# Performance work log

Measured on AMD Instinct MI355X. Metric: run time of the kernel, lower is better.

Reference implementation:

```python
import jax, jax.numpy as jnp
import numpy as np

BANDWIDTH = 1.0  # init kwarg: bandwidth; sphere mode -> var_s = gamma = bandwidth
LOG2PI = float(np.log(2.0 * np.pi))


def setup_inputs() -> dict:
    key = jax.random.key(0)
    k1, k2, k3, k4 = jax.random.split(key, 4)
    x = jax.random.normal(k1, (4096, 256), dtype=jnp.float32)
    y = jax.random.normal(k2, (4096, 128), dtype=jnp.float32)
    x_s = jax.random.normal(k3, (8192, 256), dtype=jnp.float32)
    y_s = jax.random.normal(k4, (8192, 128), dtype=jnp.float32)
    return {"x": x, "y": y, "x_s": x_s, "y_s": y_s}


def _sq_dists(a, b):
    # ||a_i - b_j||^2 via GEMM expansion: (batch, num_s)
    a2 = jnp.sum(a * a, axis=-1)[:, None]
    b2 = jnp.sum(b * b, axis=-1)[None, :]
    return a2 + b2 - 2.0 * jnp.einsum("bd,sd->bs", a, b)


def reference(x, y, x_s, y_s):
    x_dim = x.shape[-1]
    y_dim = y.shape[-1]
    var_s = BANDWIDTH
    gamma = BANDWIDTH
    logA_x = x_dim * (LOG2PI + jnp.log(jnp.float32(var_s)))
    logA_y = y_dim * (LOG2PI + jnp.log(jnp.float32(gamma)))

    sdx = _sq_dists(x, x_s) / var_s  # (batch, num_s)
    sdy = _sq_dists(y, y_s) / gamma  # (batch, num_s)

    E_log_pxy = jax.nn.logsumexp(-0.5 * (logA_x + logA_y + sdx + sdy), axis=-1)
    E_log_px = jax.nn.logsumexp(-0.5 * (logA_x + sdx), axis=-1)
    E_log_py = jax.nn.logsumexp(-0.5 * (logA_y + sdy), axis=-1)
    return jnp.mean(E_log_pxy - E_log_px - E_log_py)
```

## Files before the change

kernel.cpp:

```cpp
#include <hip/hip_runtime.h>
#include <hip/hip_bf16.h>
#include <stdint.h>

#define B_N 4096
#define S_N 8192
#define KX  256
#define KY  128
#define BM 128
#define BN 128

typedef __bf16 bf16x8 __attribute__((ext_vector_type(8)));
typedef float  f32x4  __attribute__((ext_vector_type(4)));

#define OFF_XH   ((size_t)0)
#define OFF_YH   ((size_t)2097152)
#define OFF_SXH  ((size_t)3145728)
#define OFF_SYH  ((size_t)7340032)
#define OFF_NX   ((size_t)9437184)
#define OFF_NY   (OFF_NX + 16384)
#define OFF_NSX  (OFF_NY + 16384)
#define OFF_NSY  (OFF_NSX + 32768)
#define OFF_PART (OFF_NSY + 32768)
#define OFF_BSUM (OFF_PART + (size_t)3*64*4096*2*4)

__device__ __forceinline__ void gl2lds16(const void* g, void* l) {
  typedef const __attribute__((address_space(1))) unsigned int* gp_t;
  typedef __attribute__((address_space(3))) unsigned int* lp_t;
  __builtin_amdgcn_global_load_lds((gp_t)g, (lp_t)l, 16, 0, 0);
}

__device__ __forceinline__ unsigned short f2bf(float f) {
  unsigned u = __builtin_bit_cast(unsigned, f);
  return (unsigned short)((u + 0x7fffu + ((u >> 16) & 1u)) >> 16);
}

__global__ __launch_bounds__(256) void conv_all(const float* __restrict__ x,
                                                const float* __restrict__ y,
                                                const float* __restrict__ xs,
                                                const float* __restrict__ ys,
                                                char* __restrict__ ws) {
  int b    = blockIdx.x;
  int wave = threadIdx.x >> 6;
  int lane = threadIdx.x & 63;
  if (b == 0 && threadIdx.x < 2) ((unsigned*)(ws + OFF_BSUM))[threadIdx.x] = 0u;
  const float* src; unsigned short* hi; float* nrm;
  int K, r0;
  if (b < 256) {
    src = x;  hi = (unsigned short*)(ws + OFF_XH);
    nrm = (float*)(ws + OFF_NX);  K = 256; r0 = b * 16 + wave * 4;
  } else if (b < 512) {
    src = y;  hi = (unsigned short*)(ws + OFF_YH);
    nrm = (float*)(ws + OFF_NY);  K = 128; r0 = (b - 256) * 16 + wave * 4;
  } else if (b < 1024) {
    src = xs; hi = (unsigned short*)(ws + OFF_SXH);
    nrm = (float*)(ws + OFF_NSX); K = 256; r0 = (b - 512) * 16 + wave * 4;
  } else {
    src = ys; hi = (unsigned short*)(ws + OFF_SYH);
    nrm = (float*)(ws + OFF_NSY); K = 128; r0 = (b - 1024) * 16 + wave * 4;
  }
  if (K == 256) {
    float4 v[4];
    #pragma unroll
    for (int j = 0; j < 4; ++j)
      v[j] = ((const float4*)(src + (size_t)(r0 + j) * 256))[lane];
    #pragma unroll
    for (int j = 0; j < 4; ++j) {
      float vv[4] = {v[j].x, v[j].y, v[j].z, v[j].w};
      ushort4 h4;
      unsigned short* hp = (unsigned short*)&h4;
      float acc = 0.f;
      #pragma unroll
      for (int k = 0; k < 4; ++k) {
        hp[k] = f2bf(vv[k]);
        acc = fmaf(vv[k], vv[k], acc);
      }
      ((ushort4*)(hi + (size_t)(r0 + j) * 256))[lane] = h4;
      #pragma unroll
      for (int o = 32; o > 0; o >>= 1) acc += __shfl_down(acc, o);
      if (lane == 0) nrm[r0 + j] = acc;
    }
  } else {
    float2 v[4];
    #pragma unroll
    for (int j = 0; j < 4; ++j)
      v[j] = ((const float2*)(src + (size_t)(r0 + j) * 128))[lane];
    #pragma unroll
    for (int j = 0; j < 4; ++j) {
      float vv[2] = {v[j].x, v[j].y};
      ushort2 h2;
      unsigned short* hp = (unsigned short*)&h2;
      float acc = 0.f;
      #pragma unroll
      for (int k = 0; k < 2; ++k) {
        hp[k] = f2bf(vv[k]);
        acc = fmaf(vv[k], vv[k], acc);
      }
      ((ushort2*)(hi + (size_t)(r0 + j) * 128))[lane] = h2;
      #pragma unroll
      for (int o = 32; o > 0; o >>= 1) acc += __shfl_down(acc, o);
      if (lane == 0) nrm[r0 + j] = acc;
    }
  }
}

__global__ __launch_bounds__(512, 4) void mie_main(const char* __restrict__ ws,
                                                   float* __restrict__ part) {
  __shared__ __align__(16) char smem[65536];

  const int tid  = threadIdx.x;
  const int lane = tid & 63;
  const int wave = tid >> 6;
  const int c    = lane & 15;
  const int q    = lane >> 4;
  const int wm   = wave >> 1;
  const int wn   = wave & 1;

  const int b     = blockIdx.x;
  const int xcd   = b & 7;
  const int w     = b >> 3;
  const int bm_t  = w & 31;
  const int sn_t  = xcd * 8 + (w >> 5);
  const int bm0   = bm_t * BM;
  const int sn0   = sn_t * BN;

  const char* xh  = ws + OFF_XH;
  const char* yh  = ws + OFF_YH;
  const char* sxh = ws + OFF_SXH;
  const char* syh = ws + OFF_SYH;
  const float* nx  = (const float*)(ws + OFF_NX);
  const float* ny  = (const float*)(ws + OFF_NY);
  const float* nsx = (const float*)(ws + OFF_NSX);
  const float* nsy = (const float*)(ws + OFF_NSY);

  const int r  = tid >> 2;
  const int sg = (tid & 3) ^ ((r >> 1) & 3);
  const char* aXp = xh  + (size_t)(bm0 + r) * 512 + sg * 16;
  const char* aYp = yh  + (size_t)(bm0 + r) * 256 + sg * 16;
  const char* bXp = sxh + (size_t)(sn0 + r) * 512 + sg * 16;
  const char* bYp = syh + (size_t)(sn0 + r) * 256 + sg * 16;
  char* sdst = smem + wave * 1024;

  const int slot  = (q ^ ((c >> 1) & 3)) * 16;
  const int aoff0 = (wm * 32 +  0 + c) * 64 + slot;
  const int aoff1 = (wm * 32 + 16 + c) * 64 + slot;
  const int boff0 = (wn * 64 +  0 + c) * 64 + slot;
  const int boff1 = (wn * 64 + 16 + c) * 64 + slot;
  const int boff2 = (wn * 64 + 32 + c) * 64 + slot;
  const int boff3 = (wn * 64 + 48 + c) * 64 + slot;

  f32x4 accx[2][4], accy[2][4];
  #pragma unroll
  for (int i = 0; i < 2; ++i)
    #pragma unroll
    for (int j = 0; j < 4; ++j) {
      accx[i][j] = (f32x4){0.f,0.f,0.f,0.f};
      accy[i][j] = (f32x4){0.f,0.f,0.f,0.f};
    }

#define STAGE(kc) do {                                                      \
    const char* _sa; const char* _sb;                                       \
    if ((kc) < 8) { _sa = aXp + (kc) * 64;       _sb = bXp + (kc) * 64; }   \
    else          { _sa = aYp + ((kc) - 8) * 64; _sb = bYp + ((kc) - 8) * 64; } \
    char* _d = sdst + ((kc) & 3) * 16384;                                   \
    gl2lds16(_sa, _d);                                                      \
    gl2lds16(_sb, _d + 8192);                                               \
  } while (0)

#define MFMA8(ACC, A0, A1, B0, B1, B2, B3) do {                                   \
    ACC[0][0] = __builtin_amdgcn_mfma_f32_16x16x32_bf16(A0, B0, ACC[0][0], 0,0,0); \
    ACC[0][1] = __builtin_amdgcn_mfma_f32_16x16x32_bf16(A0, B1, ACC[0][1], 0,0,0); \
    ACC[0][2] = __builtin_amdgcn_mfma_f32_16x16x32_bf16(A0, B2, ACC[0][2], 0,0,0); \
    ACC[0][3] = __builtin_amdgcn_mfma_f32_16x16x32_bf16(A0, B3, ACC[0][3], 0,0,0); \
    ACC[1][0] = __builtin_amdgcn_mfma_f32_16x16x32_bf16(A1, B0, ACC[1][0], 0,0,0); \
    ACC[1][1] = __builtin_amdgcn_mfma_f32_16x16x32_bf16(A1, B1, ACC[1][1], 0,0,0); \
    ACC[1][2] = __builtin_amdgcn_mfma_f32_16x16x32_bf16(A1, B2, ACC[1][2], 0,0,0); \
    ACC[1][3] = __builtin_amdgcn_mfma_f32_16x16x32_bf16(A1, B3, ACC[1][3], 0,0,0); \
  } while (0)

#define ITER(kc, vm, ACC) do {                                              \
    asm volatile("s_waitcnt vmcnt(" #vm ")" ::: "memory");                  \
    __builtin_amdgcn_s_barrier();                                           \
    asm volatile("" ::: "memory");                                          \
    const char* _base = smem + ((kc) & 3) * 16384;                          \
    bf16x8 _A0 = *(const bf16x8*)(_base + aoff0);                           \
    bf16x8 _A1 = *(const bf16x8*)(_base + aoff1);                           \
    bf16x8 _B0 = *(const bf16x8*)(_base + 8192 + boff0);                    \
    bf16x8 _B1 = *(const bf16x8*)(_base + 8192 + boff1);                    \
    bf16x8 _B2 = *(const bf16x8*)(_base + 8192 + boff2);                    \
    bf16x8 _B3 = *(const bf16x8*)(_base + 8192 + boff3);                    \
    if ((kc) + 3 < 12) STAGE((kc) + 3);                                     \
    __builtin_amdgcn_s_setprio(1);                                          \
    MFMA8(ACC, _A0, _A1, _B0, _B1, _B2, _B3);                               \
    __builtin_amdgcn_s_setprio(0);                                          \
  } while (0)

  STAGE(0); STAGE(1); STAGE(2);

  ITER(0, 4, accx);  ITER(1, 4, accx);  ITER(2, 4, accx);  ITER(3, 4, accx);
  ITER(4, 4, accx);  ITER(5, 4, accx);  ITER(6, 4, accx);  ITER(7, 4, accx);
  ITER(8, 4, accy);  ITER(9, 4, accy);  ITER(10, 2, accy); ITER(11, 0, accy);

#undef ITER
#undef MFMA8
#undef STAGE

  __syncthreads();

  float hxv[2][4], hyv[2][4];
  #pragma unroll
  for (int i = 0; i < 2; ++i)
    #pragma unroll
    for (int rr4 = 0; rr4 < 4; ++rr4) {
      int rr = bm0 + wm * 32 + i * 16 + q * 4 + rr4;
      hxv[i][rr4] = -0.5f * nx[rr];
      hyv[i][rr4] = -0.5f * ny[rr];
    }
  float hsxv[4], hsyv[4];
  #pragma unroll
  for (int j = 0; j < 4; ++j) {
    int cc = sn0 + wn * 64 + j * 16 + c;
    hsxv[j] = -0.5f * nsx[cc];
    hsyv[j] = -0.5f * nsy[cc];
  }

  float2* xch2 = (float2*)smem;
  #pragma unroll
  for (int i = 0; i < 2; ++i) {
    #pragma unroll
    for (int rr4 = 0; rr4 < 4; ++rr4) {
      float vx[4], vy[4];
      #pragma unroll
      for (int j = 0; j < 4; ++j) {
        vx[j] = accx[i][j][rr4] + hxv[i][rr4] + hsxv[j];
        vy[j] = accy[i][j][rr4] + hyv[i][rr4] + hsyv[j];
      }
      int rl = wm * 32 + i * 16 + q * 4 + rr4;
      #pragma unroll
      for (int st = 0; st < 3; ++st) {
        float v0 = (st == 0) ? vx[0] + vy[0] : (st == 1 ? vx[0] : vy[0]);
        float v1 = (st == 0) ? vx[1] + vy[1] : (st == 1 ? vx[1] : vy[1]);
        float v2 = (st == 0) ? vx[2] + vy[2] : (st == 1 ? vx[2] : vy[2]);
        float v3 = (st == 0) ? vx[3] + vy[3] : (st == 1 ? vx[3] : vy[3]);
        float m = fmaxf(fmaxf(v0, v1), fmaxf(v2, v3));
        float s = __expf(v0 - m) + __expf(v1 - m) + __expf(v2 - m) + __expf(v3 - m);
        float mo = __shfl_xor(m, 8);
        float so = __shfl_xor(s, 8);
        float nm = fmaxf(m, mo);
        float ns = s * __expf(m - nm) + so * __expf(mo - nm);
        if (c < 8) xch2[(st * 128 + rl) * 16 + wn * 8 + c] = (float2){nm, ns};
      }
    }
  }
  __syncthreads();

  if (tid < 384) {
    int st = tid >> 7;
    int rl = tid & 127;
    const float2* row = xch2 + (st * 128 + rl) * 16;
    int p0 = rl & 15;
    float2 a = row[p0];
    float m = a.x, s = a.y;
    #pragma unroll
    for (int p = 1; p < 16; ++p) {
      float2 e = row[(p0 + p) & 15];
      float nm = fmaxf(m, e.x);
      s = s * __expf(m - nm) + e.y * __expf(e.x - nm);
      m = nm;
    }
    size_t idx = ((size_t)st * 64 + sn_t) * B_N + (bm0 + rl);
    ((float2*)part)[idx] = (float2){m, s};
  }
}

__global__ __launch_bounds__(256) void fin_all(const float* __restrict__ part,
                                               char* __restrict__ ws,
                                               float* __restrict__ out) {
  __shared__ float2 lds[3][4][64];
  int tid  = threadIdx.x;
  int wave = tid >> 6;
  int lane = tid & 63;
  int row  = blockIdx.x * 64 + lane;
  #pragma unroll
  for (int j = 0; j < 3; ++j) {
    float m = -__builtin_inff(), s = 0.f;
    #pragma unroll
    for (int pp = 0; pp < 16; ++pp) {
      int p = wave * 16 + pp;
      float2 a = ((const float2*)part)[((size_t)j * 64 + p) * B_N + row];
      float nm = fmaxf(m, a.x);
      s = s * __expf(m - nm) + a.y * __expf(a.x - nm);
      m = nm;
    }
    lds[j][wave][lane] = (float2){m, s};
  }
  __syncthreads();
  if (wave == 0) {
    float v[3];
    #pragma unroll
    for (int j = 0; j < 3; ++j) {
      float m = -__builtin_inff(), s = 0.f;
      #pragma unroll
      for (int u = 0; u < 4; ++u) {
        float2 a = lds[j][u][lane];
        float nm = fmaxf(m, a.x);
        s = s * __expf(m - nm) + a.y * __expf(a.x - nm);
        m = nm;
      }
      v[j] = m + __logf(s);
    }
    float local = v[0] - v[1] - v[2];
    #pragma unroll
    for (int o = 32; o > 0; o >>= 1) local += __shfl_down(local, o);
    if (lane == 0) {
      unsigned* done = (unsigned*)(ws + OFF_BSUM);
      float*    fsum = (float*)(done + 1);
      atomicAdd(fsum, local);
      __threadfence();
      unsigned old = atomicAdd(done, 1u);
      if (old == 63u) {
        __threadfence();
        float tot = atomicAdd(fsum, 0.0f);
        out[0] = tot * (1.0f / (float)B_N);
      }
    }
  }
}

extern "C" void kernel_launch(void* const* d_in, const int* in_sizes, int n_in,
                              void* d_out, int out_size, void* d_ws, size_t ws_size,
                              hipStream_t stream) {
  (void)in_sizes; (void)n_in; (void)out_size; (void)ws_size;
  const float* x  = (const float*)d_in[0];
  const float* y  = (const float*)d_in[1];
  const float* xs = (const float*)d_in[2];
  const float* ys = (const float*)d_in[3];
  char* ws = (char*)d_ws;

  conv_all<<<1536, 256, 0, stream>>>(x, y, xs, ys, ws);
  mie_main<<<2048, 512, 0, stream>>>(ws, (float*)(ws + OFF_PART));
  fin_all<<<B_N / 64, 256, 0, stream>>>((const float*)(ws + OFF_PART), ws, (float*)d_out);
}
```

Measured before the change: 129.5 us.

## Enlarge main-kernel tile to 256x128 rows for more operand reuse

Doubles the batch-row tile of the fused dual-GEMM/logsumexp kernel from 128 to 256, so each wave computes a 64x64 sub-tile with 16 MFMAs per k-step instead of 8. Staging, LDS layout, the wait counts, the epilogue reduction and the grid size are all reworked to match. This cuts global and LDS traffic per MFMA and halves the block count. The cost is more accumulator registers, 96KB of LDS and an occupancy target lowered to two blocks per CU, which reduces latency hiding.

```diff
diff --git a/kernel.cpp b/kernel.cpp
--- a/kernel.cpp
+++ b/kernel.cpp
@@ -6,7 +6,7 @@
 #define S_N 8192
 #define KX  256
 #define KY  128
-#define BM 128
+#define BM 256
 #define BN 128
 
 typedef __bf16 bf16x8 __attribute__((ext_vector_type(8)));
@@ -103,9 +103,9 @@
   }
 }
 
-__global__ __launch_bounds__(512, 4) void mie_main(const char* __restrict__ ws,
+__global__ __launch_bounds__(512, 2) void mie_main(const char* __restrict__ ws,
                                                    float* __restrict__ part) {
-  __shared__ __align__(16) char smem[65536];
+  __shared__ __align__(16) char smem[98304];
 
   const int tid  = threadIdx.x;
   const int lane = tid & 63;
@@ -118,8 +118,8 @@
   const int b     = blockIdx.x;
   const int xcd   = b & 7;
   const int w     = b >> 3;
-  const int bm_t  = w & 31;
-  const int sn_t  = xcd * 8 + (w >> 5);
+  const int bm_t  = w & 15;
+  const int sn_t  = xcd * 8 + (w >> 4);
   const int bm0   = bm_t * BM;
   const int sn0   = sn_t * BN;
 
@@ -132,25 +132,24 @@
   const float* nsx = (const float*)(ws + OFF_NSX);
   const float* nsy = (const float*)(ws + OFF_NSY);
 
-  const int r  = tid >> 2;
-  const int sg = (tid & 3) ^ ((r >> 1) & 3);
-  const char* aXp = xh  + (size_t)(bm0 + r) * 512 + sg * 16;
-  const char* aYp = yh  + (size_t)(bm0 + r) * 256 + sg * 16;
-  const char* bXp = sxh + (size_t)(sn0 + r) * 512 + sg * 16;
-  const char* bYp = syh + (size_t)(sn0 + r) * 256 + sg * 16;
+  const int rA = tid >> 2;
+  const int sg = (tid & 3) ^ ((rA >> 1) & 3);
+  const char* aXp = xh  + (size_t)(bm0 + rA) * 512 + sg * 16;
+  const char* aYp = yh  + (size_t)(bm0 + rA) * 256 + sg * 16;
+  const char* bXp = sxh + (size_t)(sn0 + rA) * 512 + sg * 16;
+  const char* bYp = syh + (size_t)(sn0 + rA) * 256 + sg * 16;
   char* sdst = smem + wave * 1024;
 
-  const int slot  = (q ^ ((c >> 1) & 3)) * 16;
-  const int aoff0 = (wm * 32 +  0 + c) * 64 + slot;
-  const int aoff1 = (wm * 32 + 16 + c) * 64 + slot;
-  const int boff0 = (wn * 64 +  0 + c) * 64 + slot;
-  const int boff1 = (wn * 64 + 16 + c) * 64 + slot;
-  const int boff2 = (wn * 64 + 32 + c) * 64 + slot;
-  const int boff3 = (wn * 64 + 48 + c) * 64 + slot;
-
-  f32x4 accx[2][4], accy[2][4];
-  #pragma unroll
-  for (int i = 0; i < 2; ++i)
+  const int slot = (q ^ ((c >> 1) & 3)) * 16;
+  int aoff[4], boff[4];
+  #pragma unroll
+  for (int i = 0; i < 4; ++i) aoff[i] = (wm * 64 + i * 16 + c) * 64 + slot;
+  #pragma unroll
+  for (int j = 0; j < 4; ++j) boff[j] = 16384 + (wn * 64 + j * 16 + c) * 64 + slot;
+
+  f32x4 accx[4][4], accy[4][4];
+  #pragma unroll
+  for (int i = 0; i < 4; ++i)
     #pragma unroll
     for (int j = 0; j < 4; ++j) {
       accx[i][j] = (f32x4){0.f,0.f,0.f,0.f};
@@ -158,15 +157,19 @@
     }
 
 #define STAGE(kc) do {                                                      \
-    const char* _sa; const char* _sb;                                       \
-    if ((kc) < 8) { _sa = aXp + (kc) * 64;       _sb = bXp + (kc) * 64; }   \
-    else          { _sa = aYp + ((kc) - 8) * 64; _sb = bYp + ((kc) - 8) * 64; } \
-    char* _d = sdst + ((kc) & 3) * 16384;                                   \
-    gl2lds16(_sa, _d);                                                      \
-    gl2lds16(_sb, _d + 8192);                                               \
+    char* _d = sdst + ((kc) & 3) * 24576;                                   \
+    if ((kc) < 8) {                                                         \
+      gl2lds16(aXp + (kc) * 64,         _d);                                \
+      gl2lds16(aXp + 65536 + (kc) * 64, _d + 8192);                         \
+      gl2lds16(bXp + (kc) * 64,         _d + 16384);                        \
+    } else {                                                                \
+      gl2lds16(aYp + ((kc) - 8) * 64,         _d);                          \
+      gl2lds16(aYp + 32768 + ((kc) - 8) * 64, _d + 8192);                   \
+      gl2lds16(bYp + ((kc) - 8) * 64,         _d + 16384);                  \
+    }                                                                       \
   } while (0)
 
-#define MFMA8(ACC, A0, A1, B0, B1, B2, B3) do {                                   \
+#define MFMA16(ACC, A0, A1, A2, A3, B0, B1, B2, B3) do {                          \
     ACC[0][0] = __builtin_amdgcn_mfma_f32_16x16x32_bf16(A0, B0, ACC[0][0], 0,0,0); \
     ACC[0][1] = __builtin_amdgcn_mfma_f32_16x16x32_bf16(A0, B1, ACC[0][1], 0,0,0); \
     ACC[0][2] = __builtin_amdgcn_mfma_f32_16x16x32_bf16(A0, B2, ACC[0][2], 0,0,0); \
@@ -175,46 +178,47 @@
     ACC[1][1] = __builtin_amdgcn_mfma_f32_16x16x32_bf16(A1, B1, ACC[1][1], 0,0,0); \
     ACC[1][2] = __builtin_amdgcn_mfma_f32_16x16x32_bf16(A1, B2, ACC[1][2], 0,0,0); \
     ACC[1][3] = __builtin_amdgcn_mfma_f32_16x16x32_bf16(A1, B3, ACC[1][3], 0,0,0); \
+    ACC[2][0] = __builtin_amdgcn_mfma_f32_16x16x32_bf16(A2, B0, ACC[2][0], 0,0,0); \
+    ACC[2][1] = __builtin_amdgcn_mfma_f32_16x16x32_bf16(A2, B1, ACC[2][1], 0,0,0); \
+    ACC[2][2] = __builtin_amdgcn_mfma_f32_16x16x32_bf16(A2, B2, ACC[2][2], 0,0,0); \
+    ACC[2][3] = __builtin_amdgcn_mfma_f32_16x16x32_bf16(A2, B3, ACC[2][3], 0,0,0); \
+    ACC[3][0] = __builtin_amdgcn_mfma_f32_16x16x32_bf16(A3, B0, ACC[3][0], 0,0,0); \
+    ACC[3][1] = __builtin_amdgcn_mfma_f32_16x16x32_bf16(A3, B1, ACC[3][1], 0,0,0); \
+    ACC[3][2] = __builtin_amdgcn_mfma_f32_16x16x32_bf16(A3, B2, ACC[3][2], 0,0,0); \
+    ACC[3][3] = __builtin_amdgcn_mfma_f32_16x16x32_bf16(A3, B3, ACC[3][3], 0,0,0); \
   } while (0)
 
 #define ITER(kc, vm, ACC) do {                                              \
     asm volatile("s_waitcnt vmcnt(" #vm ")" ::: "memory");                  \
     __builtin_amdgcn_s_barrier();                                           \
     asm volatile("" ::: "memory");                                          \
-    const char* _base = smem + ((kc) & 3) * 16384;                          \
-    bf16x8 _A0 = *(const bf16x8*)(_base + aoff0);                           \
-    bf16x8 _A1 = *(const bf16x8*)(_base + aoff1);                           \
-    bf16x8 _B0 = *(const bf16x8*)(_base + 8192 + boff0);                    \
-    bf16x8 _B1 = *(const bf16x8*)(_base + 8192 + boff1);                    \
-    bf16x8 _B2 = *(const bf16x8*)(_base + 8192 + boff2);                    \
-    bf16x8 _B3 = *(const bf16x8*)(_base + 8192 + boff3);                    \
+    const char* _base = smem + ((kc) & 3) * 24576;                          \
+    bf16x8 _A0 = *(const bf16x8*)(_base + aoff[0]);                         \
+    bf16x8 _A1 = *(const bf16x8*)(_base + aoff[1]);                         \
+    bf16x8 _A2 = *(const bf16x8*)(_base + aoff[2]);                         \
+    bf16x8 _A3 = *(const bf16x8*)(_base + aoff[3]);                         \
+    bf16x8 _B0 = *(const bf16x8*)(_base + boff[0]);                         \
+    bf16x8 _B1 = *(const bf16x8*)(_base + boff[1]);                         \
+    bf16x8 _B2 = *(const bf16x8*)(_base + boff[2]);                         \
+    bf16x8 _B3 = *(const bf16x8*)(_base + boff[3]);                         \
     if ((kc) + 3 < 12) STAGE((kc) + 3);                                     \
     __builtin_amdgcn_s_setprio(1);                                          \
-    MFMA8(ACC, _A0, _A1, _B0, _B1, _B2, _B3);                               \
+    MFMA16(ACC, _A0, _A1, _A2, _A3, _B0, _B1, _B2, _B3);                    \
     __builtin_amdgcn_s_setprio(0);                                          \
   } while (0)
 
   STAGE(0); STAGE(1); STAGE(2);
 
-  ITER(0, 4, accx);  ITER(1, 4, accx);  ITER(2, 4, accx);  ITER(3, 4, accx);
-  ITER(4, 4, accx);  ITER(5, 4, accx);  ITER(6, 4, accx);  ITER(7, 4, accx);
-  ITER(8, 4, accy);  ITER(9, 4, accy);  ITER(10, 2, accy); ITER(11, 0, accy);
+  ITER(0, 6, accx);  ITER(1, 6, accx);  ITER(2, 6, accx);  ITER(3, 6, accx);
+  ITER(4, 6, accx);  ITER(5, 6, accx);  ITER(6, 6, accx);  ITER(7, 6, accx);
+  ITER(8, 6, accy);  ITER(9, 6, accy);  ITER(10, 3, accy); ITER(11, 0, accy);
 
 #undef ITER
-#undef MFMA8
+#undef MFMA16
 #undef STAGE
 
   __syncthreads();
 
-  float hxv[2][4], hyv[2][4];
-  #pragma unroll
-  for (int i = 0; i < 2; ++i)
-    #pragma unroll
-    for (int rr4 = 0; rr4 < 4; ++rr4) {
-      int rr = bm0 + wm * 32 + i * 16 + q * 4 + rr4;
-      hxv[i][rr4] = -0.5f * nx[rr];
-      hyv[i][rr4] = -0.5f * ny[rr];
-    }
   float hsxv[4], hsyv[4];
   #pragma unroll
   for (int j = 0; j < 4; ++j) {
@@ -225,16 +229,18 @@
 
   float2* xch2 = (float2*)smem;
   #pragma unroll
-  for (int i = 0; i < 2; ++i) {
+  for (int i = 0; i < 4; ++i) {
     #pragma unroll
     for (int rr4 = 0; rr4 < 4; ++rr4) {
+      int rowg = wm * 64 + i * 16 + q * 4 + rr4;
+      float hx = -0.5f * nx[bm0 + rowg];
+      float hy = -0.5f * ny[bm0 + rowg];
       float vx[4], vy[4];
       #pragma unroll
       for (int j = 0; j < 4; ++j) {
-        vx[j] = accx[i][j][rr4] + hxv[i][rr4] + hsxv[j];
-        vy[j] = accy[i][j][rr4] + hyv[i][rr4] + hsyv[j];
-      }
-      int rl = wm * 32 + i * 16 + q * 4 + rr4;
+        vx[j] = accx[i][j][rr4] + hx + hsxv[j];
+        vy[j] = accy[i][j][rr4] + hy + hsyv[j];
+      }
       #pragma unroll
       for (int st = 0; st < 3; ++st) {
         float v0 = (st == 0) ? vx[0] + vy[0] : (st == 1 ? vx[0] : vy[0]);
@@ -247,16 +253,16 @@
         float so = __shfl_xor(s, 8);
         float nm = fmaxf(m, mo);
         float ns = s * __expf(m - nm) + so * __expf(mo - nm);
-        if (c < 8) xch2[(st * 128 + rl) * 16 + wn * 8 + c] = (float2){nm, ns};
+        if (c < 8) xch2[(st * 256 + rowg) * 16 + wn * 8 + c] = (float2){nm, ns};
       }
     }
   }
   __syncthreads();
 
-  if (tid < 384) {
-    int st = tid >> 7;
-    int rl = tid & 127;
-    const float2* row = xch2 + (st * 128 + rl) * 16;
+  for (int pid = tid; pid < 768; pid += 512) {
+    int st = pid >> 8;
+    int rl = pid & 255;
+    const float2* row = xch2 + (st * 256 + rl) * 16;
     int p0 = rl & 15;
     float2 a = row[p0];
     float m = a.x, s = a.y;
@@ -337,6 +343,6 @@
   char* ws = (char*)d_ws;
 
   conv_all<<<1536, 256, 0, stream>>>(x, y, xs, ys, ws);
-  mie_main<<<2048, 512, 0, stream>>>(ws, (float*)(ws + OFF_PART));
+  mie_main<<<1024, 512, 0, stream>>>(ws, (float*)(ws + OFF_PART));
   fin_all<<<B_N / 64, 256, 0, stream>>>((const float*)(ws + OFF_PART), ws, (float*)d_out);
 }
```

New measurement: 142.1 us. 9.7% more time.
